# Kernel optimization log

Hardware: AMD Instinct MI355X
Metric: run time of the kernel (lower is better)

The kernel has to match this reference:

```python
import jax, jax.numpy as jnp
import numpy as np

B, L, D, H = 2, 2048, 2048, 16
HD = D // H          # head_dim = 128
LD = HD // 4         # latent_dim = 32


def _linear_params(key, fan_in, fan_out):
    kw, kb = jax.random.split(key)
    bound = 1.0 / np.sqrt(fan_in)
    W = jax.random.uniform(kw, (fan_in, fan_out), jnp.float32, -bound, bound)
    b = jax.random.uniform(kb, (fan_out,), jnp.float32, -bound, bound)
    return W, b


def setup_inputs() -> dict:
    key = jax.random.key(0)
    ks = jax.random.split(key, 12)
    x = jax.random.normal(ks[0], (B, L, D), jnp.float32)
    cos = jax.random.uniform(ks[1], (L, HD // 2), jnp.float32)
    sin = jax.random.uniform(ks[2], (L, HD // 2), jnp.float32)
    Wq, bq = _linear_params(ks[3], D, D)
    Wk, bk = _linear_params(ks[4], D, D)
    Wv, bv = _linear_params(ks[5], D, D)
    Wqc, bqc = _linear_params(ks[6], HD, LD)
    Wkc, bkc = _linear_params(ks[7], HD, LD)
    Wvc, bvc = _linear_params(ks[8], HD, LD)
    Wd, bd = _linear_params(ks[9], LD, HD)
    Wo, bo = _linear_params(ks[10], D, D)
    return dict(x=x, cos=cos, sin=sin, Wq=Wq, bq=bq, Wk=Wk, bk=bk, Wv=Wv, bv=bv,
                Wqc=Wqc, bqc=bqc, Wkc=Wkc, bkc=bkc, Wvc=Wvc, bvc=bvc,
                Wd=Wd, bd=bd, Wo=Wo, bo=bo)


def _apply_rope(q, k, cos, sin):
    # q, k: (B, H, L, HD); cos, sin: (L, HD//2) -> broadcast over B, H
    c = cos[None, None, :, :]
    s = sin[None, None, :, :]
    qe, qo = q[..., ::2], q[..., 1::2]
    ke, ko = k[..., ::2], k[..., 1::2]
    q_rot = jnp.stack([qe * c - qo * s, qe * s + qo * c], axis=-1).reshape(q.shape)
    k_rot = jnp.stack([ke * c - ko * s, ke * s + ko * c], axis=-1).reshape(k.shape)
    return q_rot, k_rot


def reference(x, cos, sin, Wq, bq, Wk, bk, Wv, bv,
              Wqc, bqc, Wkc, bkc, Wvc, bvc, Wd, bd, Wo, bo):
    b, l, d = x.shape
    # projections -> (B, H, L, HD)
    q = (x @ Wq + bq).reshape(b, l, H, HD).transpose(0, 2, 1, 3)
    k = (x @ Wk + bk).reshape(b, l, H, HD).transpose(0, 2, 1, 3)
    v = (x @ Wv + bv).reshape(b, l, H, HD).transpose(0, 2, 1, 3)
    q, k = _apply_rope(q, k, cos, sin)
    # low-rank compression into latent_dim
    qc = jnp.einsum('bhld,de->bhle', q, Wqc) + bqc
    kc = jnp.einsum('bhld,de->bhle', k, Wkc) + bkc
    vc = jnp.einsum('bhld,de->bhle', v, Wvc) + bvc
    scores = jnp.einsum('bhqe,bhke->bhqk', qc, kc) / np.sqrt(LD).astype(np.float32)
    causal = jnp.tril(jnp.ones((l, l), dtype=bool))  # True = keep
    scores = jnp.where(causal[None, None], scores, -jnp.inf)
    probs = jax.nn.softmax(scores, axis=-1)
    attn = jnp.einsum('bhqk,bhke->bhqe', probs, vc)
    attn = jnp.einsum('bhle,ed->bhld', attn, Wd) + bd  # decompress to HD
    attn = attn.transpose(0, 2, 1, 3).reshape(b, l, d)
    return attn @ Wo + bo
```

## Files before the change

### kernel.cpp

```cpp
#include <hip/hip_runtime.h>
#include <hip/hip_bf16.h>


#define Bsz 2
#define Lseq 2048
#define Dmod 2048
#define Hn 16
#define HDim 128
#define LDim 32

typedef __bf16 bf16x8 __attribute__((ext_vector_type(8)));
typedef float f32x4 __attribute__((ext_vector_type(4)));
typedef __hip_bfloat16 bf16;

#define GLDS16(g, l)                                                    \
  __builtin_amdgcn_global_load_lds(                                     \
      (const __attribute__((address_space(1))) unsigned int*)(g),       \
      (__attribute__((address_space(3))) unsigned int*)(l), 16, 0, 0)

#define SM_COS 0
#define SM_SIN 131072
#define SM_WC 262144
#define SM_BC 274432
#define SM_WD 274528
#define SM_BD 278624
#define SM_BO 278752
#define SM_BQKV 280800
#define SM_TOT 286944

__global__ void detect_dtype(const ushort* __restrict__ x, int* __restrict__ flag) {
  int t = threadIdx.x;
  int bad = 0;
  for (int k = 0; k < 4; ++k) {
    ushort u = x[t * 4 + k];
    int ex = (u >> 7) & 0xFF;
    if (ex >= 0xC0) bad = 1;
  }
  unsigned long long b = __ballot(bad);
  if (t == 0) *flag = (b != 0ULL) ? 1 : 0;
}

__device__ inline void conv8(const void* src, size_t so, bf16* dst, size_t dof, int f32) {
  if (f32) {
    const float* s = (const float*)src + so;
    bf16 tmp[8] __attribute__((aligned(16)));
    for (int j = 0; j < 8; ++j) tmp[j] = __float2bfloat16(s[j]);
    *(uint4*)&dst[dof] = *(uint4*)tmp;
  } else {
    *(uint4*)&dst[dof] = *(const uint4*)((const ushort*)src + so);
  }
}

__device__ inline float cv1(const void* s, size_t i, int f32) {
  return f32 ? ((const float*)s)[i] : __bfloat162float(((const bf16*)s)[i]);
}

#define NB_T3 3072
#define NB_WV 2048
#define NB_CX 4096
#define NB_PREP 160
#define NB_FBP 256
#define NB_PREP_ALL (NB_T3 + NB_WV + NB_CX + NB_PREP + NB_FBP)

__global__ __launch_bounds__(256) void prep_all(
    const void* xS, const void* cosS, const void* sinS, const void* WqS,
    const void* WkS, const void* WvS, const void* WoS, const void* WqcS,
    const void* WkcS, const void* WvcS, const void* bqcS, const void* bkcS,
    const void* bvcS, const void* WdS, const void* bdS, const void* boS,
    const void* bqS, const void* bkS, const void* bvS,
    bf16* __restrict__ xb, bf16* __restrict__ WvB, bf16* __restrict__ WtQK,
    bf16* __restrict__ WtO, bf16* __restrict__ small, bf16* __restrict__ wctG,
    bf16* __restrict__ wdtG, float* __restrict__ bo_part,
    const int* __restrict__ flagp) {
  __shared__ __align__(16) char shm[16640];
  int f32 = *flagp;
  int blk = blockIdx.x;
  int t = threadIdx.x;

  if (blk < NB_T3) {
    float (*tile)[65] = (float(*)[65])shm;
    int z = blk >> 10, rem = blk & 1023;
    const void* W = (z == 0) ? WqS : (z == 1) ? WkS : WoS;
    bf16* Wt = (z == 2) ? WtO : (WtQK + (size_t)z * 2048 * 2048);
    int n0 = (rem & 31) * 64, k0 = (rem >> 5) * 64;
    int x = (t & 7) * 8, y = t >> 3;
    for (int p = 0; p < 2; ++p) {
      int r = y + p * 32;
      if (f32) {
        const float* src = (const float*)W + (size_t)(k0 + r) * 2048 + n0 + x;
        float4 a = *(const float4*)src;
        float4 b2 = *(const float4*)(src + 4);
        tile[r][x + 0] = a.x; tile[r][x + 1] = a.y; tile[r][x + 2] = a.z; tile[r][x + 3] = a.w;
        tile[r][x + 4] = b2.x; tile[r][x + 5] = b2.y; tile[r][x + 6] = b2.z; tile[r][x + 7] = b2.w;
      } else {
        const ushort* src = (const ushort*)W + (size_t)(k0 + r) * 2048 + n0 + x;
        uint4 u = *(const uint4*)src;
        bf16* e = (bf16*)&u;
        for (int jj = 0; jj < 8; ++jj) tile[r][x + jj] = __bfloat162float(e[jj]);
      }
    }
    __syncthreads();
    for (int p = 0; p < 2; ++p) {
      int n = y + p * 32;
      bf16 tmp[8] __attribute__((aligned(16)));
      for (int jj = 0; jj < 8; ++jj) tmp[jj] = __float2bfloat16(tile[x + jj][n]);
      *(uint4*)&Wt[(size_t)(n0 + n) * 2048 + k0 + x] = *(uint4*)tmp;
    }
  } else if (blk < NB_T3 + NB_WV) {
    size_t e = ((size_t)(blk - NB_T3) * 256 + t) * 8;
    conv8(WvS, e, WvB, e, f32);
  } else if (blk < NB_T3 + NB_WV + NB_CX) {
    size_t e = ((size_t)(blk - NB_T3 - NB_WV) * 256 + t) * 8;
    conv8(xS, e, xb, e, f32);
  } else if (blk < NB_T3 + NB_WV + NB_CX + NB_PREP) {
    int tid = (blk - NB_T3 - NB_WV - NB_CX) * 256 + t;
    if (tid < SM_TOT / 8) {
      size_t e = (size_t)tid * 8;
      const void* src;
      size_t so;
      if (e < SM_SIN) { src = cosS; so = e - SM_COS; }
      else if (e < SM_WC) { src = sinS; so = e - SM_SIN; }
      else if (e < SM_BC) { size_t r = e - SM_WC; src = (r < 4096) ? WqcS : (r < 8192) ? WkcS : WvcS; so = r & 4095; }
      else if (e < SM_WD) { size_t r = e - SM_BC; src = (r < 32) ? bqcS : (r < 64) ? bkcS : bvcS; so = r & 31; }
      else if (e < SM_BD) { src = WdS; so = e - SM_WD; }
      else if (e < SM_BO) { src = bdS; so = e - SM_BD; }
      else if (e < SM_BQKV) { src = boS; so = e - SM_BO; }
      else { size_t r = e - SM_BQKV; src = (r < 2048) ? bqS : (r < 4096) ? bkS : bvS; so = r & 2047; }
      conv8(src, so, small, e, f32);
    } else {
      int idx = tid - SM_TOT / 8;
      for (int i = idx; i < 16384; i += 40960 - SM_TOT / 8) {
        if (i < 12288) {
          int reg = i >> 12, rem2 = i & 4095, n = rem2 >> 7, k = rem2 & 127;
          const void* src = (reg == 0) ? WqcS : (reg == 1) ? WkcS : WvcS;
          wctG[i] = __float2bfloat16(cv1(src, (size_t)k * 32 + n, f32));
        } else {
          int i2 = i - 12288, o = i2 >> 5, e = i2 & 31;
          wdtG[i2] = __float2bfloat16(cv1(WdS, (size_t)e * 128 + o, f32));
        }
      }
    }
  } else {
    float* red = (float*)shm;
    int rem = blk - (NB_T3 + NB_WV + NB_CX + NB_PREP);
    int nb = rem & 15, kb = rem >> 4;
    int col = nb * 128 + (t & 127);
    int half = t >> 7;
    float s = 0.f;
    int kbase = kb * 128 + half * 64;
    for (int i = 0; i < 64; ++i) {
      int k = kbase + i;
      s += cv1(bdS, k & 127, f32) * cv1(WoS, (size_t)k * 2048 + col, f32);
    }
    red[t] = s;
    __syncthreads();
    if (half == 0) bo_part[kb * 2048 + col] = red[t] + red[t + 128];
  }
}

__global__ __launch_bounds__(256) void fold_all(
    const bf16* __restrict__ WvB, const bf16* __restrict__ wctG,
    const bf16* __restrict__ WtO, const bf16* __restrict__ small,
    const void* boS, const float* __restrict__ bo_part, const void* bvS,
    const void* bvcS, const void* WvcS, bf16* __restrict__ Wvt,
    bf16* __restrict__ Wot, float* __restrict__ boF, float* __restrict__ bvF,
    const int* __restrict__ flagp) {
  int blk = blockIdx.x;
  int t = threadIdx.x, lane = t & 63, w = t >> 6;
  int qd = lane >> 4, ln = lane & 15;
  if (blk < 256) {
    int nb = blk & 15, h = blk >> 4;
    f32x4 acc[2][2] = {};
    for (int kt = 0; kt < 4; ++kt) {
      bf16x8 af[2], bfr[2];
      for (int i = 0; i < 2; ++i)
        af[i] = *(const bf16x8*)&wctG[8192 + (i * 16 + ln) * 128 + kt * 32 + qd * 8];
      for (int j = 0; j < 2; ++j)
        bfr[j] = *(const bf16x8*)&WvB[(size_t)(nb * 128 + w * 32 + j * 16 + ln) * 2048 +
                                      h * 128 + kt * 32 + qd * 8];
      for (int i = 0; i < 2; ++i)
        for (int j = 0; j < 2; ++j)
          acc[i][j] = __builtin_amdgcn_mfma_f32_16x16x32_bf16(af[i], bfr[j], acc[i][j], 0, 0, 0);
    }
    for (int i = 0; i < 2; ++i)
      for (int j = 0; j < 2; ++j)
        for (int r = 0; r < 4; ++r) {
          int e = i * 16 + qd * 4 + r;
          int col = nb * 128 + w * 32 + j * 16 + ln;
          Wvt[(size_t)(h * 32 + e) * 2048 + col] = __float2bfloat16(acc[i][j][r]);
        }
  } else if (blk < 512) {
    int rem = blk - 256;
    int mb = rem & 15, h = rem >> 4;
    f32x4 acc[2][2] = {};
    for (int kt = 0; kt < 4; ++kt) {
      bf16x8 af[2], bfr[2];
      for (int i = 0; i < 2; ++i)
        af[i] = *(const bf16x8*)&WtO[(size_t)(mb * 128 + w * 32 + i * 16 + ln) * 2048 +
                                     h * 128 + kt * 32 + qd * 8];
      for (int j = 0; j < 2; ++j)
        bfr[j] = *(const bf16x8*)&small[SM_WD + (j * 16 + ln) * 128 + kt * 32 + qd * 8];
      for (int i = 0; i < 2; ++i)
        for (int j = 0; j < 2; ++j)
          acc[i][j] = __builtin_amdgcn_mfma_f32_16x16x32_bf16(af[i], bfr[j], acc[i][j], 0, 0, 0);
    }
    for (int i = 0; i < 2; ++i)
      for (int j = 0; j < 2; ++j)
        for (int r = 0; r < 4; ++r) {
          int row = mb * 128 + w * 32 + i * 16 + qd * 4 + r;
          int col = h * 32 + j * 16 + ln;
          Wot[(size_t)row * 512 + col] = __float2bfloat16(acc[i][j][r]);
        }
  } else {
    int f32 = *flagp;
    int tid = (blk - 512) * 256 + t;
    if (tid < 2048) {
      float s = cv1(boS, tid, f32);
      for (int kb = 0; kb < 16; ++kb) s += bo_part[kb * 2048 + tid];
      boF[tid] = s;
    } else if (tid < 2560) {
      int j = tid - 2048, h = j >> 5, e = j & 31;
      float s = cv1(bvcS, e, f32);
      for (int hd = 0; hd < 128; ++hd)
        s += cv1(bvS, h * 128 + hd, f32) * cv1(WvcS, (size_t)hd * 32 + e, f32);
      bvF[j] = s;
    }
  }
}

#define ESTR 136
__global__ __launch_bounds__(256) void gemm_qkv(
    const bf16* __restrict__ A, const bf16* __restrict__ Bt,
    const bf16* __restrict__ Wvt, const bf16* __restrict__ small,
    const bf16* __restrict__ wctG, const float* __restrict__ bvF,
    bf16* __restrict__ qc, bf16* __restrict__ kc, bf16* __restrict__ vcT) {
  __shared__ bf16 sh[128 * ESTR];
  const int K = 2048;
  int id = blockIdx.x;
  int t = threadIdx.x;
  int lane = t & 63, w = t >> 6;
  int qd = lane >> 4, ln = lane & 15;

  if (id < 1024) {
    bf16* lA = sh;
    bf16* lB = sh + 4096;
    int bn = id & 31, bm = id >> 5;
    int reg = bn >> 4, h = bn & 15;
    int wm = (w >> 1) * 64, wn = (w & 1) * 64;

    f32x4 acc[4][4] = {};
    const bf16* Ab = A + (size_t)(bm * 128) * K;
    const bf16* Bb = Bt + (size_t)(bn * 128) * K;

    for (int kt = 0; kt < K; kt += 32) {
      for (int p = 0; p < 2; ++p) {
        int slot = t + p * 256;
        int r = slot >> 2, c = (slot & 3) * 8;
        GLDS16(&Ab[(size_t)r * K + kt + c], &lA[slot * 8]);
        GLDS16(&Bb[(size_t)r * K + kt + c], &lB[slot * 8]);
      }
      __syncthreads();
      bf16x8 af[4], bfr[4];
      for (int i = 0; i < 4; ++i) af[i] = *(bf16x8*)&lA[(wm + i * 16 + ln) * 32 + qd * 8];
      for (int j = 0; j < 4; ++j) bfr[j] = *(bf16x8*)&lB[(wn + j * 16 + ln) * 32 + qd * 8];
      for (int i = 0; i < 4; ++i)
        for (int j = 0; j < 4; ++j)
          acc[i][j] = __builtin_amdgcn_mfma_f32_16x16x32_bf16(af[i], bfr[j], acc[i][j], 0, 0, 0);
      __syncthreads();
    }

    for (int j = 0; j < 4; ++j) {
      int col = wn + j * 16 + ln;
      float bv = __bfloat162float(small[SM_BQKV + bn * 128 + col]);
      for (int i = 0; i < 4; ++i)
        for (int r = 0; r < 4; ++r)
          sh[(wm + i * 16 + qd * 4 + r) * ESTR + col] = __float2bfloat16(acc[i][j][r] + bv);
    }
    __syncthreads();

    int r0 = w * 32;
    int b = bm >> 4;
    int bh = b * Hn + h;
    bf16x8 bfr2[2][4];
    for (int nt = 0; nt < 2; ++nt)
      for (int kt = 0; kt < 4; ++kt)
        bfr2[nt][kt] = *(const bf16x8*)&wctG[reg * 4096 + (nt * 16 + ln) * 128 + kt * 32 + qd * 8];
    float bc[2];
    bc[0] = __bfloat162float(small[SM_BC + reg * 32 + ln]);
    bc[1] = __bfloat162float(small[SM_BC + reg * 32 + 16 + ln]);

    for (int mt = 0; mt < 2; ++mt) {
      int lb = r0 + mt * 16 + ln;
      int lg2 = (bm & 15) * 128 + lb;
      f32x4 c2[2] = {};
      for (int kt = 0; kt < 4; ++kt) {
        uint4 u = *(uint4*)&sh[lb * ESTR + kt * 32 + qd * 8];
        bf16* e8 = (bf16*)&u;
        int pbase = kt * 16 + qd * 4;
        uint2 cu = *(const uint2*)&small[SM_COS + (size_t)lg2 * 64 + pbase];
        uint2 su = *(const uint2*)&small[SM_SIN + (size_t)lg2 * 64 + pbase];
        const bf16* cp = (const bf16*)&cu;
        const bf16* sp = (const bf16*)&su;
        for (int j = 0; j < 4; ++j) {
          float cvv = __bfloat162float(cp[j]);
          float svv = __bfloat162float(sp[j]);
          float ev = __bfloat162float(e8[2 * j]);
          float ov = __bfloat162float(e8[2 * j + 1]);
          e8[2 * j] = __float2bfloat16(ev * cvv - ov * svv);
          e8[2 * j + 1] = __float2bfloat16(ev * svv + ov * cvv);
        }
        bf16x8 a = *(bf16x8*)&u;
        c2[0] = __builtin_amdgcn_mfma_f32_16x16x32_bf16(a, bfr2[0][kt], c2[0], 0, 0, 0);
        c2[1] = __builtin_amdgcn_mfma_f32_16x16x32_bf16(a, bfr2[1][kt], c2[1], 0, 0, 0);
      }
      int lgbase = (bm & 15) * 128 + r0 + mt * 16 + qd * 4;
      bf16* dst = (reg == 0) ? qc : kc;
      for (int nt = 0; nt < 2; ++nt)
        for (int r = 0; r < 4; ++r)
          dst[((size_t)bh * Lseq + lgbase + r) * 32 + nt * 16 + ln] =
              __float2bfloat16(c2[nt][r] + bc[nt]);
    }
  } else {
    bf16* lA = sh;
    bf16* lB = sh + 2048;
    int rem = id - 1024;
    int nb = rem & 7, bm = rem >> 3;
    int wm = (w >> 1) * 32, wn = (w & 1) * 32;

    f32x4 acc[2][2] = {};
    const bf16* Ab = A + (size_t)(bm * 64) * K;
    const bf16* Bb = Wvt + (size_t)(nb * 64) * K;

    int r = t >> 2, c = (t & 3) * 8;
    for (int kt = 0; kt < K; kt += 32) {
      GLDS16(&Ab[(size_t)r * K + kt + c], &lA[t * 8]);
      GLDS16(&Bb[(size_t)r * K + kt + c], &lB[t * 8]);
      __syncthreads();
      bf16x8 af[2], bfr[2];
      for (int i = 0; i < 2; ++i) af[i] = *(bf16x8*)&lA[(wm + i * 16 + ln) * 32 + qd * 8];
      for (int j = 0; j < 2; ++j) bfr[j] = *(bf16x8*)&lB[(wn + j * 16 + ln) * 32 + qd * 8];
      for (int i = 0; i < 2; ++i)
        for (int j = 0; j < 2; ++j)
          acc[i][j] = __builtin_amdgcn_mfma_f32_16x16x32_bf16(af[i], bfr[j], acc[i][j], 0, 0, 0);
      __syncthreads();
    }

    int b = bm >> 5;
    for (int j = 0; j < 2; ++j) {
      int n = nb * 64 + wn + j * 16 + ln;
      float bb = bvF[n];
      for (int i = 0; i < 2; ++i) {
        int lloc = (bm & 31) * 64 + wm + i * 16 + qd * 4;
        bf16 p4[4] __attribute__((aligned(8)));
        for (int rr = 0; rr < 4; ++rr) p4[rr] = __float2bfloat16(acc[i][j][rr] + bb);
        *(uint2*)&vcT[((size_t)(b * 512 + n)) * 2048 + lloc] = *(uint2*)p4;
      }
    }
  }
}

__global__ __launch_bounds__(256) void gemm_bias_out(const bf16* __restrict__ A,
                                                     const bf16* __restrict__ Bt,
                                                     const float* __restrict__ bias,
                                                     void* __restrict__ C,
                                                     int M, int N, int K,
                                                     const int* __restrict__ flagp) {
  __shared__ bf16 lA[128 * 32];
  __shared__ bf16 lB[128 * 32];
  int f32out = *flagp;
  int bm = blockIdx.y, bn = blockIdx.x;
  int t = threadIdx.x;
  int lane = t & 63, w = t >> 6;
  int wm = (w >> 1) * 64, wn = (w & 1) * 64;
  int qd = lane >> 4, ln = lane & 15;

  f32x4 acc[4][4] = {};
  const bf16* Ab = A + (size_t)(bm * 128) * K;
  const bf16* Bb = Bt + (size_t)(bn * 128) * K;

  for (int kt = 0; kt < K; kt += 32) {
    for (int p = 0; p < 2; ++p) {
      int slot = t + p * 256;
      int r = slot >> 2, c = (slot & 3) * 8;
      GLDS16(&Ab[(size_t)r * K + kt + c], &lA[slot * 8]);
      GLDS16(&Bb[(size_t)r * K + kt + c], &lB[slot * 8]);
    }
    __syncthreads();
    bf16x8 af[4], bfr[4];
    for (int i = 0; i < 4; ++i) af[i] = *(bf16x8*)&lA[(wm + i * 16 + ln) * 32 + qd * 8];
    for (int j = 0; j < 4; ++j) bfr[j] = *(bf16x8*)&lB[(wn + j * 16 + ln) * 32 + qd * 8];
    for (int i = 0; i < 4; ++i)
      for (int j = 0; j < 4; ++j)
        acc[i][j] = __builtin_amdgcn_mfma_f32_16x16x32_bf16(af[i], bfr[j], acc[i][j], 0, 0, 0);
    __syncthreads();
  }
  for (int i = 0; i < 4; ++i)
    for (int j = 0; j < 4; ++j) {
      int col = bn * 128 + wn + j * 16 + ln;
      float bv = bias[col];
      for (int r = 0; r < 4; ++r) {
        int row = bm * 128 + wm + i * 16 + qd * 4 + r;
        float v = acc[i][j][r] + bv;
        if (f32out) ((float*)C)[(size_t)row * N + col] = v;
        else ((bf16*)C)[(size_t)row * N + col] = __float2bfloat16(v);
      }
    }
}

__global__ __launch_bounds__(256) void flash32(const bf16* __restrict__ qc,
                                               const bf16* __restrict__ kc,
                                               const bf16* __restrict__ vcT,
                                               bf16* __restrict__ attn) {
  __shared__ bf16 pbuf[4][16 * 72];
  __shared__ float oL[4][16][33];
  __shared__ float mL[4][16];
  __shared__ float lsL[4][16];
  int t = threadIdx.x;
  int lane = t & 63, w = t >> 6;
  int qd = lane >> 4, ln = lane & 15;
  int blk = blockIdx.x;
  int j = blk & 127;
  int bh = blk >> 7, h = bh & 15, b = bh >> 4;
  int q0 = j * 16;

  bf16x8 qf = *(const bf16x8*)&qc[((size_t)bh * Lseq + q0 + ln) * 32 + qd * 8];

  f32x4 o0 = {}, o1 = {};
  float m[4], ls[4];
  for (int r = 0; r < 4; ++r) { m[r] = -1e30f; ls[r] = 0.f; }
  const float scale2 = 0.17677669529663687f * 1.4426950408889634f;

  int n64 = (q0 + 16 + 63) >> 6;
  int nw = (n64 + 3) >> 2;
  int c0 = w * nw;
  int c1 = min(c0 + nw, n64);

  bf16* pb = pbuf[w];
  bf16x8 kf[4];
  if (c0 < c1) {
    int k0 = c0 * 64;
    for (int c = 0; c < 4; ++c)
      kf[c] = *(const bf16x8*)&kc[((size_t)bh * Lseq + k0 + c * 16 + ln) * 32 + qd * 8];
  }
  for (int ci = c0; ci < c1; ++ci) {
    int k0 = ci * 64;
    f32x4 s[4];
    for (int c = 0; c < 4; ++c) {
      f32x4 z = {};
      s[c] = __builtin_amdgcn_mfma_f32_16x16x32_bf16(qf, kf[c], z, 0, 0, 0);
    }
    size_t vbase = ((size_t)bh * 32 + ln) * Lseq + k0 + qd * 8;
    bf16x8 vf00 = *(const bf16x8*)&vcT[vbase];
    bf16x8 vf01 = *(const bf16x8*)&vcT[vbase + 32];
    bf16x8 vf10 = *(const bf16x8*)&vcT[vbase + (size_t)16 * Lseq];
    bf16x8 vf11 = *(const bf16x8*)&vcT[vbase + (size_t)16 * Lseq + 32];
    if (ci + 1 < c1) {
      int k0n = k0 + 64;
      for (int c = 0; c < 4; ++c)
        kf[c] = *(const bf16x8*)&kc[((size_t)bh * Lseq + k0n + c * 16 + ln) * 32 + qd * 8];
    }
    float sv[4][4], alpha[4];
    for (int r = 0; r < 4; ++r) {
      int qrow = q0 + qd * 4 + r;
      for (int c = 0; c < 4; ++c)
        sv[c][r] = (k0 + c * 16 + ln <= qrow) ? s[c][r] * scale2 : -1e30f;
    }
    for (int r = 0; r < 4; ++r) {
      float mx = fmaxf(fmaxf(sv[0][r], sv[1][r]), fmaxf(sv[2][r], sv[3][r]));
      for (int off = 1; off < 16; off <<= 1) mx = fmaxf(mx, __shfl_xor(mx, off, 64));
      float mn = fmaxf(m[r], mx);
      alpha[r] = exp2f(m[r] - mn);
      m[r] = mn;
      float rs = 0.f;
      for (int c = 0; c < 4; ++c) { sv[c][r] = exp2f(sv[c][r] - mn); rs += sv[c][r]; }
      ls[r] = ls[r] * alpha[r] + rs;
      o0[r] *= alpha[r];
      o1[r] *= alpha[r];
    }
    for (int r = 0; r < 4; ++r)
      for (int c = 0; c < 4; ++c)
        pb[(qd * 4 + r) * 72 + c * 16 + ln] = __float2bfloat16(sv[c][r]);
    asm volatile("s_waitcnt lgkmcnt(0)" ::: "memory");
    bf16x8 pf0 = *(bf16x8*)&pb[ln * 72 + qd * 8];
    bf16x8 pf1 = *(bf16x8*)&pb[ln * 72 + 32 + qd * 8];
    o0 = __builtin_amdgcn_mfma_f32_16x16x32_bf16(pf0, vf00, o0, 0, 0, 0);
    o0 = __builtin_amdgcn_mfma_f32_16x16x32_bf16(pf1, vf01, o0, 0, 0, 0);
    o1 = __builtin_amdgcn_mfma_f32_16x16x32_bf16(pf0, vf10, o1, 0, 0, 0);
    o1 = __builtin_amdgcn_mfma_f32_16x16x32_bf16(pf1, vf11, o1, 0, 0, 0);
  }

  for (int r = 0; r < 4; ++r)
    for (int off = 1; off < 16; off <<= 1) ls[r] += __shfl_xor(ls[r], off, 64);

  for (int r = 0; r < 4; ++r) {
    int row = qd * 4 + r;
    oL[w][row][ln] = o0[r];
    oL[w][row][16 + ln] = o1[r];
    if (ln == 0) { mL[w][row] = m[r]; lsL[w][row] = ls[r]; }
  }
  __syncthreads();

  for (int idx = t; idx < 512; idx += 256) {
    int row = idx >> 5, col = idx & 31;
    float m0 = mL[0][row], m1 = mL[1][row], m2 = mL[2][row], m3 = mL[3][row];
    float ms = fmaxf(fmaxf(m0, m1), fmaxf(m2, m3));
    float e0 = exp2f(m0 - ms), e1 = exp2f(m1 - ms);
    float e2 = exp2f(m2 - ms), e3 = exp2f(m3 - ms);
    float lsum = lsL[0][row] * e0 + lsL[1][row] * e1 + lsL[2][row] * e2 + lsL[3][row] * e3;
    float val = oL[0][row][col] * e0 + oL[1][row][col] * e1 +
                oL[2][row][col] * e2 + oL[3][row][col] * e3;
    int l = q0 + row;
    attn[((size_t)(b * Lseq + l)) * 512 + h * 32 + col] = __float2bfloat16(val / lsum);
  }
}

extern "C" void kernel_launch(void* const* d_in, const int* in_sizes, int n_in,
                              void* d_out, int out_size, void* d_ws, size_t ws_size,
                              hipStream_t stream) {
  const void* x = d_in[0];
  const void* cosS = d_in[1];
  const void* sinS = d_in[2];
  const void* Wq = d_in[3];
  const void* bq = d_in[4];
  const void* Wk = d_in[5];
  const void* bk = d_in[6];
  const void* Wv = d_in[7];
  const void* bv = d_in[8];
  const void* Wqc = d_in[9];
  const void* bqc = d_in[10];
  const void* Wkc = d_in[11];
  const void* bkc = d_in[12];
  const void* Wvc = d_in[13];
  const void* bvc = d_in[14];
  const void* Wd = d_in[15];
  const void* bd = d_in[16];
  const void* Wo = d_in[17];
  const void* bo = d_in[18];

  char* ws = (char*)d_ws;
  size_t off = 0;
  auto alloc = [&](size_t bytes) {
    char* p = ws + off;
    off += (bytes + 255) & ~(size_t)255;
    return p;
  };
  int* flag = (int*)alloc(256);
  bf16* small = (bf16*)alloc((size_t)SM_TOT * 2);
  bf16* wctG = (bf16*)alloc((size_t)12288 * 2);
  bf16* wdtG = (bf16*)alloc((size_t)4096 * 2);
  bf16* xb = (bf16*)alloc((size_t)4096 * 2048 * 2);
  bf16* WvB = (bf16*)alloc((size_t)2048 * 2048 * 2);
  bf16* WtQK = (bf16*)alloc((size_t)4096 * 2048 * 2);
  bf16* WtO = (bf16*)alloc((size_t)2048 * 2048 * 2);
  bf16* Wvt = (bf16*)alloc((size_t)512 * 2048 * 2);
  bf16* Wot = (bf16*)alloc((size_t)2048 * 512 * 2);
  float* bo_part = (float*)alloc((size_t)16 * 2048 * 4);
  float* boF = (float*)alloc((size_t)2048 * 4);
  float* bvF = (float*)alloc((size_t)512 * 4);
  bf16* qcW = (bf16*)alloc((size_t)65536 * 32 * 2);
  bf16* kcW = (bf16*)alloc((size_t)65536 * 32 * 2);
  bf16* vcTW = (bf16*)alloc((size_t)65536 * 32 * 2);
  bf16* attnW = (bf16*)alloc((size_t)4096 * 512 * 2);

  dim3 tb(256);
  detect_dtype<<<1, 64, 0, stream>>>((const ushort*)x, flag);
  prep_all<<<NB_PREP_ALL, tb, 0, stream>>>(
      x, cosS, sinS, Wq, Wk, Wv, Wo, Wqc, Wkc, Wvc, bqc, bkc, bvc, Wd, bd, bo,
      bq, bk, bv, xb, WvB, WtQK, WtO, small, wctG, wdtG, bo_part, flag);
  fold_all<<<522, tb, 0, stream>>>(WvB, wctG, WtO, small, bo, bo_part, bv, bvc,
                                   Wvc, Wvt, Wot, boF, bvF, flag);
  gemm_qkv<<<1536, tb, 0, stream>>>(xb, WtQK, Wvt, small, wctG, bvF, qcW, kcW, vcTW);
  flash32<<<4096, tb, 0, stream>>>(qcW, kcW, vcTW, attnW);
  gemm_bias_out<<<dim3(16, 32), tb, 0, stream>>>(attnW, Wot, boF, d_out, 4096, 2048,
                                                 512, flag);
}
```

Before: 394.2 us.

## Fold Wv/Wo low-rank products directly in prep kernel, drop fold_all launch

The Wv·Wvc and Wd·Wo weight folds are now computed directly from the source weights inside prep_all using scalar FMA with shared-memory staging. This removes the intermediate bf16 copies of Wv and transposed Wo and the separate fold_all kernel launch. The boF reduction moves into extra blocks of gemm_qkv. The folds now use scalar FP32 arithmetic instead of MFMA, which does more ALU work per block and reads the source weights uncoalesced or more than once.

```diff
diff --git a/kernel.cpp b/kernel.cpp
--- a/kernel.cpp
+++ b/kernel.cpp
@@ -55,12 +55,14 @@
   return f32 ? ((const float*)s)[i] : __bfloat162float(((const bf16*)s)[i]);
 }
 
-#define NB_T3 3072
-#define NB_WV 2048
-#define NB_CX 4096
-#define NB_PREP 160
-#define NB_FBP 256
-#define NB_PREP_ALL (NB_T3 + NB_WV + NB_CX + NB_PREP + NB_FBP)
+#define PB_T2 0
+#define PB_CX 2048
+#define PB_PREP 6144
+#define PB_FBP 6304
+#define PB_FVW 6560
+#define PB_FOW 7072
+#define PB_BVF 7328
+#define NB_PREP_ALL 7330
 
 __global__ __launch_bounds__(256) void prep_all(
     const void* xS, const void* cosS, const void* sinS, const void* WqS,
@@ -68,20 +70,20 @@
     const void* WkcS, const void* WvcS, const void* bqcS, const void* bkcS,
     const void* bvcS, const void* WdS, const void* bdS, const void* boS,
     const void* bqS, const void* bkS, const void* bvS,
-    bf16* __restrict__ xb, bf16* __restrict__ WvB, bf16* __restrict__ WtQK,
-    bf16* __restrict__ WtO, bf16* __restrict__ small, bf16* __restrict__ wctG,
-    bf16* __restrict__ wdtG, float* __restrict__ bo_part,
+    bf16* __restrict__ xb, bf16* __restrict__ WtQK, bf16* __restrict__ small,
+    bf16* __restrict__ wctG, float* __restrict__ bo_part,
+    bf16* __restrict__ Wvt, bf16* __restrict__ Wot, float* __restrict__ bvF,
     const int* __restrict__ flagp) {
-  __shared__ __align__(16) char shm[16640];
+  __shared__ __align__(16) char shm[16896];
   int f32 = *flagp;
   int blk = blockIdx.x;
   int t = threadIdx.x;
 
-  if (blk < NB_T3) {
+  if (blk < PB_CX) {
     float (*tile)[65] = (float(*)[65])shm;
     int z = blk >> 10, rem = blk & 1023;
-    const void* W = (z == 0) ? WqS : (z == 1) ? WkS : WoS;
-    bf16* Wt = (z == 2) ? WtO : (WtQK + (size_t)z * 2048 * 2048);
+    const void* W = (z == 0) ? WqS : WkS;
+    bf16* Wt = WtQK + (size_t)z * 2048 * 2048;
     int n0 = (rem & 31) * 64, k0 = (rem >> 5) * 64;
     int x = (t & 7) * 8, y = t >> 3;
     for (int p = 0; p < 2; ++p) {
@@ -106,14 +108,11 @@
       for (int jj = 0; jj < 8; ++jj) tmp[jj] = __float2bfloat16(tile[x + jj][n]);
       *(uint4*)&Wt[(size_t)(n0 + n) * 2048 + k0 + x] = *(uint4*)tmp;
     }
-  } else if (blk < NB_T3 + NB_WV) {
-    size_t e = ((size_t)(blk - NB_T3) * 256 + t) * 8;
-    conv8(WvS, e, WvB, e, f32);
-  } else if (blk < NB_T3 + NB_WV + NB_CX) {
-    size_t e = ((size_t)(blk - NB_T3 - NB_WV) * 256 + t) * 8;
+  } else if (blk < PB_PREP) {
+    size_t e = ((size_t)(blk - PB_CX) * 256 + t) * 8;
     conv8(xS, e, xb, e, f32);
-  } else if (blk < NB_T3 + NB_WV + NB_CX + NB_PREP) {
-    int tid = (blk - NB_T3 - NB_WV - NB_CX) * 256 + t;
+  } else if (blk < PB_FBP) {
+    int tid = (blk - PB_PREP) * 256 + t;
     if (tid < SM_TOT / 8) {
       size_t e = (size_t)tid * 8;
       const void* src;
@@ -129,20 +128,15 @@
       conv8(src, so, small, e, f32);
     } else {
       int idx = tid - SM_TOT / 8;
-      for (int i = idx; i < 16384; i += 40960 - SM_TOT / 8) {
-        if (i < 12288) {
-          int reg = i >> 12, rem2 = i & 4095, n = rem2 >> 7, k = rem2 & 127;
-          const void* src = (reg == 0) ? WqcS : (reg == 1) ? WkcS : WvcS;
-          wctG[i] = __float2bfloat16(cv1(src, (size_t)k * 32 + n, f32));
-        } else {
-          int i2 = i - 12288, o = i2 >> 5, e = i2 & 31;
-          wdtG[i2] = __float2bfloat16(cv1(WdS, (size_t)e * 128 + o, f32));
-        }
+      for (int i = idx; i < 12288; i += 40960 - SM_TOT / 8) {
+        int reg = i >> 12, rem2 = i & 4095, n = rem2 >> 7, k = rem2 & 127;
+        const void* src = (reg == 0) ? WqcS : (reg == 1) ? WkcS : WvcS;
+        wctG[i] = __float2bfloat16(cv1(src, (size_t)k * 32 + n, f32));
       }
     }
-  } else {
+  } else if (blk < PB_FVW) {
     float* red = (float*)shm;
-    int rem = blk - (NB_T3 + NB_WV + NB_CX + NB_PREP);
+    int rem = blk - PB_FBP;
     int nb = rem & 15, kb = rem >> 4;
     int col = nb * 128 + (t & 127);
     int half = t >> 7;
@@ -155,75 +149,59 @@
     red[t] = s;
     __syncthreads();
     if (half == 0) bo_part[kb * 2048 + col] = red[t] + red[t + 128];
-  }
-}
-
-__global__ __launch_bounds__(256) void fold_all(
-    const bf16* __restrict__ WvB, const bf16* __restrict__ wctG,
-    const bf16* __restrict__ WtO, const bf16* __restrict__ small,
-    const void* boS, const float* __restrict__ bo_part, const void* bvS,
-    const void* bvcS, const void* WvcS, bf16* __restrict__ Wvt,
-    bf16* __restrict__ Wot, float* __restrict__ boF, float* __restrict__ bvF,
-    const int* __restrict__ flagp) {
-  int blk = blockIdx.x;
-  int t = threadIdx.x, lane = t & 63, w = t >> 6;
-  int qd = lane >> 4, ln = lane & 15;
-  if (blk < 256) {
-    int nb = blk & 15, h = blk >> 4;
-    f32x4 acc[2][2] = {};
-    for (int kt = 0; kt < 4; ++kt) {
-      bf16x8 af[2], bfr[2];
-      for (int i = 0; i < 2; ++i)
-        af[i] = *(const bf16x8*)&wctG[8192 + (i * 16 + ln) * 128 + kt * 32 + qd * 8];
-      for (int j = 0; j < 2; ++j)
-        bfr[j] = *(const bf16x8*)&WvB[(size_t)(nb * 128 + w * 32 + j * 16 + ln) * 2048 +
-                                      h * 128 + kt * 32 + qd * 8];
-      for (int i = 0; i < 2; ++i)
-        for (int j = 0; j < 2; ++j)
-          acc[i][j] = __builtin_amdgcn_mfma_f32_16x16x32_bf16(af[i], bfr[j], acc[i][j], 0, 0, 0);
-    }
-    for (int i = 0; i < 2; ++i)
-      for (int j = 0; j < 2; ++j)
-        for (int r = 0; r < 4; ++r) {
-          int e = i * 16 + qd * 4 + r;
-          int col = nb * 128 + w * 32 + j * 16 + ln;
-          Wvt[(size_t)(h * 32 + e) * 2048 + col] = __float2bfloat16(acc[i][j][r]);
-        }
-  } else if (blk < 512) {
-    int rem = blk - 256;
-    int mb = rem & 15, h = rem >> 4;
-    f32x4 acc[2][2] = {};
-    for (int kt = 0; kt < 4; ++kt) {
-      bf16x8 af[2], bfr[2];
-      for (int i = 0; i < 2; ++i)
-        af[i] = *(const bf16x8*)&WtO[(size_t)(mb * 128 + w * 32 + i * 16 + ln) * 2048 +
-                                     h * 128 + kt * 32 + qd * 8];
-      for (int j = 0; j < 2; ++j)
-        bfr[j] = *(const bf16x8*)&small[SM_WD + (j * 16 + ln) * 128 + kt * 32 + qd * 8];
-      for (int i = 0; i < 2; ++i)
-        for (int j = 0; j < 2; ++j)
-          acc[i][j] = __builtin_amdgcn_mfma_f32_16x16x32_bf16(af[i], bfr[j], acc[i][j], 0, 0, 0);
-    }
-    for (int i = 0; i < 2; ++i)
-      for (int j = 0; j < 2; ++j)
-        for (int r = 0; r < 4; ++r) {
-          int row = mb * 128 + w * 32 + i * 16 + qd * 4 + r;
-          int col = h * 32 + j * 16 + ln;
-          Wot[(size_t)row * 512 + col] = __float2bfloat16(acc[i][j][r]);
-        }
+  } else if (blk < PB_FOW) {
+    float* wvc = (float*)shm;
+    for (int i = t; i < 4096; i += 256) wvc[i] = cv1(WvcS, i, f32);
+    __syncthreads();
+    int rem = blk - PB_FVW;
+    int h = rem >> 5, kb = rem & 31;
+    int k = kb * 64 + (t >> 2);
+    int e0 = (t & 3) * 8;
+    float acc[8] = {};
+    for (int hd0 = 0; hd0 < 128; hd0 += 8) {
+      float wv[8];
+      for (int j = 0; j < 8; ++j)
+        wv[j] = cv1(WvS, (size_t)k * 2048 + h * 128 + hd0 + j, f32);
+      for (int j = 0; j < 8; ++j)
+        for (int e = 0; e < 8; ++e)
+          acc[e] += wv[j] * wvc[(hd0 + j) * 32 + e0 + e];
+    }
+    for (int e = 0; e < 8; ++e)
+      Wvt[(size_t)(h * 32 + e0 + e) * 2048 + k] = __float2bfloat16(acc[e]);
+  } else if (blk < PB_BVF) {
+    float* wd = (float*)shm;
+    for (int i = t; i < 4096; i += 256) wd[i] = cv1(WdS, i, f32);
+    __syncthreads();
+    int rem = blk - PB_FOW;
+    int h = rem >> 4, db = rem & 15;
+    int d = db * 128 + (t & 127);
+    int half = t >> 7;
+    float acc[32] = {};
+    for (int hd = half * 64; hd < half * 64 + 64; ++hd) {
+      float wo = cv1(WoS, (size_t)(h * 128 + hd) * 2048 + d, f32);
+      for (int e = 0; e < 32; ++e) acc[e] += wd[e * 128 + hd] * wo;
+    }
+    __syncthreads();
+    float* xch = (float*)shm;
+    if (half) {
+      for (int e = 0; e < 32; ++e) xch[(t & 127) * 33 + e] = acc[e];
+    }
+    __syncthreads();
+    if (!half) {
+      bf16 out[32] __attribute__((aligned(16)));
+      for (int e = 0; e < 32; ++e)
+        out[e] = __float2bfloat16(acc[e] + xch[(t & 127) * 33 + e]);
+      for (int q = 0; q < 4; ++q)
+        *(uint4*)&Wot[(size_t)d * 512 + h * 32 + q * 8] = *(uint4*)&out[q * 8];
+    }
   } else {
-    int f32 = *flagp;
-    int tid = (blk - 512) * 256 + t;
-    if (tid < 2048) {
-      float s = cv1(boS, tid, f32);
-      for (int kb = 0; kb < 16; ++kb) s += bo_part[kb * 2048 + tid];
-      boF[tid] = s;
-    } else if (tid < 2560) {
-      int j = tid - 2048, h = j >> 5, e = j & 31;
+    int tid = (blk - PB_BVF) * 256 + t;
+    if (tid < 512) {
+      int h = tid >> 5, e = tid & 31;
       float s = cv1(bvcS, e, f32);
       for (int hd = 0; hd < 128; ++hd)
         s += cv1(bvS, h * 128 + hd, f32) * cv1(WvcS, (size_t)hd * 32 + e, f32);
-      bvF[j] = s;
+      bvF[tid] = s;
     }
   }
 }
@@ -233,7 +211,9 @@
     const bf16* __restrict__ A, const bf16* __restrict__ Bt,
     const bf16* __restrict__ Wvt, const bf16* __restrict__ small,
     const bf16* __restrict__ wctG, const float* __restrict__ bvF,
-    bf16* __restrict__ qc, bf16* __restrict__ kc, bf16* __restrict__ vcT) {
+    const void* boS, const float* __restrict__ bo_part,
+    bf16* __restrict__ qc, bf16* __restrict__ kc, bf16* __restrict__ vcT,
+    float* __restrict__ boF, const int* __restrict__ flagp) {
   __shared__ bf16 sh[128 * ESTR];
   const int K = 2048;
   int id = blockIdx.x;
@@ -320,7 +300,7 @@
           dst[((size_t)bh * Lseq + lgbase + r) * 32 + nt * 16 + ln] =
               __float2bfloat16(c2[nt][r] + bc[nt]);
     }
-  } else {
+  } else if (id < 1536) {
     bf16* lA = sh;
     bf16* lB = sh + 2048;
     int rem = id - 1024;
@@ -356,6 +336,12 @@
         *(uint2*)&vcT[((size_t)(b * 512 + n)) * 2048 + lloc] = *(uint2*)p4;
       }
     }
+  } else {
+    int f32 = *flagp;
+    int tid = (id - 1536) * 256 + t;
+    float s = cv1(boS, tid, f32);
+    for (int kb = 0; kb < 16; ++kb) s += bo_part[kb * 2048 + tid];
+    boF[tid] = s;
   }
 }
 
@@ -547,11 +533,8 @@
   int* flag = (int*)alloc(256);
   bf16* small = (bf16*)alloc((size_t)SM_TOT * 2);
   bf16* wctG = (bf16*)alloc((size_t)12288 * 2);
-  bf16* wdtG = (bf16*)alloc((size_t)4096 * 2);
   bf16* xb = (bf16*)alloc((size_t)4096 * 2048 * 2);
-  bf16* WvB = (bf16*)alloc((size_t)2048 * 2048 * 2);
   bf16* WtQK = (bf16*)alloc((size_t)4096 * 2048 * 2);
-  bf16* WtO = (bf16*)alloc((size_t)2048 * 2048 * 2);
   bf16* Wvt = (bf16*)alloc((size_t)512 * 2048 * 2);
   bf16* Wot = (bf16*)alloc((size_t)2048 * 512 * 2);
   float* bo_part = (float*)alloc((size_t)16 * 2048 * 4);
@@ -566,10 +549,9 @@
   detect_dtype<<<1, 64, 0, stream>>>((const ushort*)x, flag);
   prep_all<<<NB_PREP_ALL, tb, 0, stream>>>(
       x, cosS, sinS, Wq, Wk, Wv, Wo, Wqc, Wkc, Wvc, bqc, bkc, bvc, Wd, bd, bo,
-      bq, bk, bv, xb, WvB, WtQK, WtO, small, wctG, wdtG, bo_part, flag);
-  fold_all<<<522, tb, 0, stream>>>(WvB, wctG, WtO, small, bo, bo_part, bv, bvc,
-                                   Wvc, Wvt, Wot, boF, bvF, flag);
-  gemm_qkv<<<1536, tb, 0, stream>>>(xb, WtQK, Wvt, small, wctG, bvF, qcW, kcW, vcTW);
+      bq, bk, bv, xb, WtQK, small, wctG, bo_part, Wvt, Wot, bvF, flag);
+  gemm_qkv<<<1544, tb, 0, stream>>>(xb, WtQK, Wvt, small, wctG, bvF, bo, bo_part,
+                                    qcW, kcW, vcTW, boF, flag);
   flash32<<<4096, tb, 0, stream>>>(qcW, kcW, vcTW, attnW);
   gemm_bias_out<<<dim3(16, 32), tb, 0, stream>>>(attnW, Wot, boF, d_out, 4096, 2048,
                                                  512, flag);
```

New measurement: 407.6 us. 3.4% more time.
